# Optimization experiments

Hardware: AMD Instinct MI355X
Metric: run time of the kernel (lower is better)

## Reference

```python
import jax, jax.numpy as jnp
import numpy as np

B, T, D_MODEL = 2, 2048, 2048
Q_HEADS, KV_HEADS = 16, 4
HEAD_DIM = D_MODEL // Q_HEADS  # 128
N_GROUPS = Q_HEADS // KV_HEADS  # 4
THETA = 10000.0


def setup_inputs() -> dict:
    key = jax.random.key(0)
    ks = jax.random.split(key, 5)
    s = 0.02
    return {
        "x": jax.random.normal(ks[0], (B, T, D_MODEL), dtype=jnp.float32),
        "Wq": jax.random.normal(ks[1], (Q_HEADS * HEAD_DIM, D_MODEL), dtype=jnp.float32) * s,
        "Wk": jax.random.normal(ks[2], (KV_HEADS * HEAD_DIM, D_MODEL), dtype=jnp.float32) * s,
        "Wv": jax.random.normal(ks[3], (KV_HEADS * HEAD_DIM, D_MODEL), dtype=jnp.float32) * s,
        "Wo": jax.random.normal(ks[4], (D_MODEL, D_MODEL), dtype=jnp.float32) * s,
    }


def _apply_rope(q, k, t):
    # freqs = outer(arange(t), 1/theta^(2i/d)) ; complex rotation on (even,odd) pairs
    inv_freq = 1.0 / (THETA ** (jnp.arange(0, HEAD_DIM, 2, dtype=jnp.float32) / HEAD_DIM))
    ang = jnp.arange(t, dtype=jnp.float32)[:, None] * inv_freq[None, :]  # [t, hd/2]
    cos = jnp.cos(ang)[None, :, None, :]  # [1,t,1,hd/2]
    sin = jnp.sin(ang)[None, :, None, :]

    def rot(x):
        xr = x.reshape(*x.shape[:-1], HEAD_DIM // 2, 2)
        xe, xo = xr[..., 0], xr[..., 1]
        out = jnp.stack([xe * cos - xo * sin, xe * sin + xo * cos], axis=-1)
        return out.reshape(x.shape)

    return rot(q), rot(k)


def reference(x, Wq, Wk, Wv, Wo):
    b, t, c = x.shape
    q = (x @ Wq.T).reshape(b, t, Q_HEADS, HEAD_DIM)
    k = (x @ Wk.T).reshape(b, t, KV_HEADS, HEAD_DIM)
    v = (x @ Wv.T).reshape(b, t, KV_HEADS, HEAD_DIM)
    q, k = _apply_rope(q, k, t)
    # GQA: repeat kv heads to match q heads (repeat_interleave on head dim)
    k = jnp.repeat(k, N_GROUPS, axis=2)
    v = jnp.repeat(v, N_GROUPS, axis=2)
    q = q.transpose(0, 2, 1, 3)  # [b,h,t,d]
    k = k.transpose(0, 2, 1, 3)
    v = v.transpose(0, 2, 1, 3)
    scale = HEAD_DIM ** -0.5
    attn = jnp.einsum("bhqd,bhkd->bhqk", q, k) * scale
    causal = jnp.tril(jnp.ones((t, t), dtype=bool))
    attn = jnp.where(causal[None, None], attn, -jnp.inf)
    attn = jax.nn.softmax(attn, axis=-1)
    out = jnp.einsum("bhqk,bhkd->bhqd", attn, v)
    out = out.transpose(0, 2, 1, 3).reshape(b, t, c)
    return out @ Wo.T
```

## Files before the change

kernel.cpp:

```cpp
#include <hip/hip_runtime.h>
#include <hip/hip_bf16.h>

typedef __bf16 bf16_t;
typedef __bf16 bf16x8 __attribute__((ext_vector_type(8)));
typedef __bf16 bf16x4 __attribute__((ext_vector_type(4)));
typedef float f32x4 __attribute__((ext_vector_type(4)));

#define SEQ_T 2048
#define DMODEL 2048
#define NQH 16
#define NKVH 4
#define HDIM 128

__device__ __forceinline__ f32x4 mfma16x16x32(bf16x8 a, bf16x8 b, f32x4 c) {
  return __builtin_amdgcn_mfma_f32_16x16x32_bf16(a, b, c, 0, 0, 0);
}

typedef __attribute__((address_space(3))) void lds_void_t;
typedef __attribute__((address_space(1))) const void gbl_void_t;
__device__ __forceinline__ void gload_lds16(const bf16_t* g, bf16_t* l) {
  __builtin_amdgcn_global_load_lds((gbl_void_t*)g, (lds_void_t*)l, 16, 0, 0);
}
__device__ __forceinline__ void BAR() {
  asm volatile("" ::: "memory");
  __builtin_amdgcn_s_barrier();
  asm volatile("" ::: "memory");
}

__global__ __launch_bounds__(256) void cast_all(const float* __restrict__ x,
                                                const float* __restrict__ Wq,
                                                const float* __restrict__ Wk,
                                                const float* __restrict__ Wv,
                                                const float* __restrict__ Wo,
                                                bf16_t* __restrict__ xb,
                                                bf16_t* __restrict__ Wqkvb,
                                                bf16_t* __restrict__ Wob) {
  const int idx = blockIdx.x * 256 + threadIdx.x;
  const float* src;
  bf16_t* dst;
  if (idx < 1048576) {
    src = x + (size_t)idx * 8;
    dst = xb + (size_t)idx * 8;
  } else if (idx < 1572864) {
    const int r = idx - 1048576;
    src = Wq + (size_t)r * 8;
    dst = Wqkvb + (size_t)r * 8;
  } else if (idx < 1703936) {
    const int r = idx - 1572864;
    src = Wk + (size_t)r * 8;
    dst = Wqkvb + 4194304 + (size_t)r * 8;
  } else if (idx < 1835008) {
    const int r = idx - 1703936;
    src = Wv + (size_t)r * 8;
    dst = Wqkvb + 5242880 + (size_t)r * 8;
  } else {
    const int r = idx - 1835008;
    src = Wo + (size_t)r * 8;
    dst = Wob + (size_t)r * 8;
  }
  const float4* s4 = reinterpret_cast<const float4*>(src);
  float4 a = s4[0], b = s4[1];
  bf16x8 r8 = {(bf16_t)a.x, (bf16_t)a.y, (bf16_t)a.z, (bf16_t)a.w,
               (bf16_t)b.x, (bf16_t)b.y, (bf16_t)b.z, (bf16_t)b.w};
  *reinterpret_cast<bf16x8*>(dst) = r8;
}

__global__ __launch_bounds__(256) void sincos_kernel(float2* __restrict__ tab) {
  int idx = blockIdx.x * 256 + threadIdx.x;
  int t = idx >> 6, i = idx & 63;
  float inv = powf(10000.0f, -(float)i * (1.0f / 64.0f));
  float ang = (float)t * inv;
  float s, c;
  sincosf(ang, &s, &c);
  tab[idx] = make_float2(c, s);
}

__global__ __launch_bounds__(512, 2) void gemm_qkv(const bf16_t* __restrict__ A,
                                                   const bf16_t* __restrict__ W,
                                                   bf16_t* __restrict__ q_out,
                                                   bf16_t* __restrict__ k_out,
                                                   bf16_t* __restrict__ v_out,
                                                   const float2* __restrict__ tab) {
  constexpr int K = 2048;
  constexpr int NT = 32;
  const int id = ((int)blockIdx.x & 7) * 32 + ((int)blockIdx.x >> 3);
  const int m0 = (id >> 4) * 256, n0 = (id & 15) * 192;
  const int tid = threadIdx.x;
  const int lane = tid & 63, w = tid >> 6;
  const int wr = w >> 2, wc = w & 3;
  const int l15 = lane & 15, g = lane >> 4;
  __shared__ bf16_t smem[2][(256 + 192) * 64];
  f32x4 acc[8][3] = {};
  bf16x8 af[4][2], bfr[3][2];

  auto ISSUE_A = [&](int tt, int h) {
    bf16_t* base = &smem[tt & 1][0] + h * (128 * 64);
    const bf16_t* src = A + (size_t)(m0 + h * 128) * K + tt * 64;
#pragma unroll
    for (int i = 0; i < 2; i++) {
      const int rl = i * 64 + (tid >> 3);
      gload_lds16(src + (size_t)rl * K + (((tid & 7) ^ (rl & 7)) << 3),
                  base + (i * 64 + w * 8) * 64);
    }
  };
  auto ISSUE_B = [&](int tt, int c) {
    bf16_t* base = &smem[tt & 1][0] + (256 + c * 64) * 64;
    const int rl = tid >> 3;
    const bf16_t* src = W + (size_t)(n0 + c * 64 + rl) * K + tt * 64;
    gload_lds16(src + (((tid & 7) ^ (rl & 7)) << 3), base + (w * 8) * 64);
  };
  auto RDA = [&](const bf16_t* Ab, int qm) {
#pragma unroll
    for (int fi = 0; fi < 4; fi++) {
      const int row = wr * 128 + qm * 64 + fi * 16 + l15;
#pragma unroll
      for (int ksl = 0; ksl < 2; ksl++)
        af[fi][ksl] = *reinterpret_cast<const bf16x8*>(
            Ab + row * 64 + ((((ksl << 2) + g) ^ (row & 7)) << 3));
    }
  };
  auto RDB1 = [&](const bf16_t* Bb, int fj) {
    const int row = wc * 48 + fj * 16 + l15;
#pragma unroll
    for (int ksl = 0; ksl < 2; ksl++)
      bfr[fj][ksl] = *reinterpret_cast<const bf16x8*>(
          Bb + row * 64 + ((((ksl << 2) + g) ^ (row & 7)) << 3));
  };

#define MMX(QM, FJLO, FJHI)                                                   \
  do {                                                                        \
    __builtin_amdgcn_s_setprio(1);                                            \
    _Pragma("unroll") for (int fi = 0; fi < 4; fi++)                          \
        _Pragma("unroll") for (int fj = (FJLO); fj <= (FJHI); fj++)           \
            _Pragma("unroll") for (int ksl = 0; ksl < 2; ksl++)               \
                acc[(QM)*4 + fi][fj] =                                        \
                    mfma16x16x32(af[fi][ksl], bfr[fj][ksl], acc[(QM)*4 + fi][fj]); \
    __builtin_amdgcn_s_setprio(0);                                            \
  } while (0)

  ISSUE_A(0, 0);
  ISSUE_A(0, 1);
  ISSUE_B(0, 0);
  ISSUE_B(0, 1);
  ISSUE_B(0, 2);

  for (int t = 0; t < NT; t++) {
    const bf16_t* Ab = &smem[t & 1][0];
    const bf16_t* Bb = Ab + 256 * 64;
    if (t + 1 < NT) {
      ISSUE_A(t + 1, 0);
      asm volatile("s_waitcnt vmcnt(2)" ::: "memory");
    } else {
      asm volatile("s_waitcnt vmcnt(0)" ::: "memory");
    }
    BAR();
    RDA(Ab, 0);
    RDB1(Bb, 0);
    RDB1(Bb, 1);
    MMX(0, 0, 1);
    BAR();
    RDB1(Bb, 2);
    if (t + 1 < NT) ISSUE_A(t + 1, 1);
    BAR();
    MMX(0, 2, 2);
    BAR();
    RDA(Ab, 1);
    if (t + 1 < NT) {
      ISSUE_B(t + 1, 0);
      ISSUE_B(t + 1, 1);
    }
    BAR();
    MMX(1, 0, 1);
    BAR();
    if (t + 1 < NT) ISSUE_B(t + 1, 2);
    BAR();
    MMX(1, 2, 2);
    BAR();
  }
#undef MMX

#pragma unroll
  for (int fm = 0; fm < 8; fm++) {
    const int r0 = m0 + wr * 128 + fm * 16 + (g << 2);
    const int bb = r0 >> 11;
    const int tt = r0 & 2047;
#pragma unroll
    for (int fn = 0; fn < 3; fn++) {
      const int col = n0 + wc * 48 + fn * 16 + l15;
      const f32x4 v = acc[fm][fn];
      if (col < 2048) {
        const int dd = col & 127;
        const float2* tp = tab + (size_t)tt * 64 + (dd >> 1);
        bf16_t* dst = q_out + (((size_t)(bb * NQH + (col >> 7)) * SEQ_T + tt) * HDIM + dd);
#pragma unroll
        for (int i = 0; i < 4; i++) {
          float me = v[i];
          float ot = __shfl_xor(me, 1);
          float2 cs = tp[(size_t)i * 64];
          float r = (dd & 1) ? (me * cs.x + ot * cs.y) : (me * cs.x - ot * cs.y);
          dst[(size_t)i * HDIM] = (bf16_t)r;
        }
      } else if (col < 2560) {
        const int dd = col & 127;
        const float2* tp = tab + (size_t)tt * 64 + (dd >> 1);
        bf16_t* dst = k_out + (((size_t)(bb * NKVH + ((col - 2048) >> 7)) * SEQ_T + tt) * HDIM + dd);
#pragma unroll
        for (int i = 0; i < 4; i++) {
          float me = v[i];
          float ot = __shfl_xor(me, 1);
          float2 cs = tp[(size_t)i * 64];
          float r = (dd & 1) ? (me * cs.x + ot * cs.y) : (me * cs.x - ot * cs.y);
          dst[(size_t)i * HDIM] = (bf16_t)r;
        }
      } else {
        const int vc = col - 2560;
        const int hh = vc >> 7, dd = vc & 127;
        const int tp64 = (tt & ~63) | (((tt >> 2) & 3) << 4) | (((tt >> 4) & 3) << 2);
        bf16x4 pk = {(bf16_t)v[0], (bf16_t)v[1], (bf16_t)v[2], (bf16_t)v[3]};
        *reinterpret_cast<bf16x4*>(v_out + (((size_t)(bb * NKVH + hh) * HDIM + dd) * SEQ_T + tp64)) = pk;
      }
    }
  }
}

__global__ __launch_bounds__(512, 2) void gemm_out(const bf16_t* __restrict__ A,
                                                   const bf16_t* __restrict__ W,
                                                   float* __restrict__ c_out) {
  constexpr int K = 2048;
  constexpr int NT = 32;
  const int id = ((int)blockIdx.x & 7) * 32 + ((int)blockIdx.x >> 3);
  const int m0 = (id >> 4) * 256, n0 = (id & 15) * 128;
  const int tid = threadIdx.x;
  const int lane = tid & 63, w = tid >> 6;
  const int wr = w >> 2, wc = w & 3;
  const int l15 = lane & 15, g = lane >> 4;
  __shared__ bf16_t smem[2][(256 + 128) * 64];
  f32x4 acc[8][2] = {};
  bf16x8 af[4][2], bfr[1][2];

  auto ISSUE_HALF = [&](int tt, int h) {
    const int k0 = tt * 64;
    bf16_t* base = &smem[tt & 1][0] + ((h < 2) ? h * (128 * 64) : 256 * 64);
    const bf16_t* src = (h < 2) ? (A + (size_t)(m0 + h * 128) * K)
                                : (W + (size_t)n0 * K);
#pragma unroll
    for (int i = 0; i < 2; i++) {
      const int rl = i * 64 + (tid >> 3);
      gload_lds16(src + (size_t)rl * K + k0 + (((tid & 7) ^ (rl & 7)) << 3),
                  base + (i * 64 + w * 8) * 64);
    }
  };
  auto RDA = [&](const bf16_t* Ab, int qm) {
#pragma unroll
    for (int fi = 0; fi < 4; fi++) {
      const int row = wr * 128 + qm * 64 + fi * 16 + l15;
#pragma unroll
      for (int ksl = 0; ksl < 2; ksl++)
        af[fi][ksl] = *reinterpret_cast<const bf16x8*>(
            Ab + row * 64 + ((((ksl << 2) + g) ^ (row & 7)) << 3));
    }
  };
  auto RDB = [&](const bf16_t* Bb, int qn) {
    const int row = wc * 32 + qn * 16 + l15;
#pragma unroll
    for (int ksl = 0; ksl < 2; ksl++)
      bfr[0][ksl] = *reinterpret_cast<const bf16x8*>(
          Bb + row * 64 + ((((ksl << 2) + g) ^ (row & 7)) << 3));
  };

#define MMPH(QM, QN)                                                          \
  do {                                                                        \
    __builtin_amdgcn_s_setprio(1);                                            \
    _Pragma("unroll") for (int fi = 0; fi < 4; fi++)                          \
        _Pragma("unroll") for (int ksl = 0; ksl < 2; ksl++)                   \
            acc[(QM)*4 + fi][(QN)] =                                          \
                mfma16x16x32(af[fi][ksl], bfr[0][ksl], acc[(QM)*4 + fi][(QN)]); \
    __builtin_amdgcn_s_setprio(0);                                            \
  } while (0)

#pragma unroll
  for (int h = 0; h < 3; h++) ISSUE_HALF(0, h);

  for (int t = 0; t < NT; t++) {
    const bf16_t* Ab = &smem[t & 1][0];
    const bf16_t* Bb = Ab + 256 * 64;
    if (t + 1 < NT) {
      ISSUE_HALF(t + 1, 0);
      asm volatile("s_waitcnt vmcnt(2)" ::: "memory");
    } else {
      asm volatile("s_waitcnt vmcnt(0)" ::: "memory");
    }
    BAR();
    RDA(Ab, 0);
    RDB(Bb, 0);
    MMPH(0, 0);
    BAR();
    RDB(Bb, 1);
    if (t + 1 < NT) ISSUE_HALF(t + 1, 1);
    BAR();
    MMPH(0, 1);
    BAR();
    RDA(Ab, 1);
    if (t + 1 < NT) ISSUE_HALF(t + 1, 2);
    BAR();
    MMPH(1, 1);
    BAR();
    RDB(Bb, 0);
    BAR();
    MMPH(1, 0);
    BAR();
  }
#undef MMPH

#pragma unroll
  for (int fm = 0; fm < 8; fm++) {
    const int r0 = m0 + wr * 128 + fm * 16 + (g << 2);
#pragma unroll
    for (int fn = 0; fn < 2; fn++) {
      const int col = n0 + wc * 32 + fn * 16 + l15;
#pragma unroll
      for (int i = 0; i < 4; i++) c_out[(size_t)(r0 + i) * 2048 + col] = acc[fm][fn][i];
    }
  }
}

__global__ __launch_bounds__(256, 2) void attn_kernel(const bf16_t* __restrict__ Qb,
                                                      const bf16_t* __restrict__ Kb,
                                                      const bf16_t* __restrict__ Vt,
                                                      bf16_t* __restrict__ AO) {
  const int bh = blockIdx.x;
  const int b = bh >> 4, h = bh & 15, kvh = h >> 2;
  const int p = blockIdx.y;
  const int jH = 31 - p, jL = p;
  const int q0H = jH * 64, q0L = jL * 64;
  const int tid = threadIdx.x;
  const int lane = tid & 63, w = tid >> 6;
  const bf16_t* Qp = Qb + (size_t)(b * NQH + h) * SEQ_T * HDIM;
  const bf16_t* Kp = Kb + (size_t)(b * NKVH + kvh) * SEQ_T * HDIM;
  const bf16_t* Vp = Vt + (size_t)(b * NKVH + kvh) * HDIM * SEQ_T;
  __shared__ bf16_t smem[2][16384];
  const int l15 = lane & 15, g = lane >> 4;
  const int qrA = q0H + w * 16 + l15;
  const int qrB = q0L + w * 16 + l15;
  bf16x8 qfA[4], qfB[4];
#pragma unroll
  for (int c = 0; c < 4; c++) {
    qfA[c] = *reinterpret_cast<const bf16x8*>(Qp + (size_t)qrA * HDIM + c * 32 + (g << 3));
    qfB[c] = *reinterpret_cast<const bf16x8*>(Qp + (size_t)qrB * HDIM + c * 32 + (g << 3));
  }
  f32x4 oA[8] = {}, oB[8] = {};
  float mA = -1e30f, lA = 0.0f, mB = -1e30f, lB = 0.0f;
  const float kscale = 0.08838834764831845f * 1.4426950408889634f;
  const int wmaxB = q0L + w * 16 + 15;
  const int ntiles = jH + 1;

  auto STAGE = [&](int it, int buf) {
    const int kv0s = it * 64;
    bf16_t* Ks = smem[buf];
    bf16_t* Vs = smem[buf] + 8192;
#pragma unroll
    for (int cc = 0; cc < 4; cc++) {
      const int ck = cc * 256 + tid;
      const int krow = ck >> 4, kg = ck & 15;
      gload_lds16(Kp + (size_t)(kv0s + krow) * HDIM + ((kg ^ (krow & 7)) << 3),
                  Ks + (cc * 256 + w * 64) * 8);
      const int vrow = ck >> 3, vg = ck & 7;
      gload_lds16(Vp + (size_t)vrow * SEQ_T + kv0s + ((vg ^ (vrow & 7)) << 3),
                  Vs + (cc * 256 + w * 64) * 8);
    }
  };

  auto SOFTMAX = [&](float* sv, float& m, float& l, f32x4* o, bf16x8* pc) {
    float a0 = fmaxf(fmaxf(sv[0], sv[1]), fmaxf(sv[2], sv[3]));
    float a1 = fmaxf(fmaxf(sv[4], sv[5]), fmaxf(sv[6], sv[7]));
    float a2 = fmaxf(fmaxf(sv[8], sv[9]), fmaxf(sv[10], sv[11]));
    float a3 = fmaxf(fmaxf(sv[12], sv[13]), fmaxf(sv[14], sv[15]));
    float tm = fmaxf(fmaxf(a0, a1), fmaxf(a2, a3));
    tm = fmaxf(tm, __shfl_xor(tm, 16, 64));
    tm = fmaxf(tm, __shfl_xor(tm, 32, 64));
    tm *= kscale;
    if (!__all(tm <= m + 8.0f)) {
      const float mnew = fmaxf(m, tm);
      const float alpha = exp2f(m - mnew);
      m = mnew;
      l *= alpha;
#pragma unroll
      for (int dt = 0; dt < 8; dt++) o[dt] *= alpha;
    }
#pragma unroll
    for (int j = 0; j < 16; j++) sv[j] = exp2f(__builtin_fmaf(sv[j], kscale, -m));
    float r0 = (sv[0] + sv[1]) + (sv[2] + sv[3]);
    float r1 = (sv[4] + sv[5]) + (sv[6] + sv[7]);
    float r2 = (sv[8] + sv[9]) + (sv[10] + sv[11]);
    float r3 = (sv[12] + sv[13]) + (sv[14] + sv[15]);
    float rs = (r0 + r1) + (r2 + r3);
    rs += __shfl_xor(rs, 16, 64);
    rs += __shfl_xor(rs, 32, 64);
    l += rs;
#pragma unroll
    for (int s = 0; s < 2; s++) {
      bf16x8 t = {(bf16_t)sv[8 * s],     (bf16_t)sv[8 * s + 1], (bf16_t)sv[8 * s + 2],
                  (bf16_t)sv[8 * s + 3], (bf16_t)sv[8 * s + 4], (bf16_t)sv[8 * s + 5],
                  (bf16_t)sv[8 * s + 6], (bf16_t)sv[8 * s + 7]};
      pc[s] = t;
    }
  };

  auto COMPUTE1 = [&](const bf16_t* Ks, const bf16_t* Vs, int kv0) {
    float sv[16];
    const bool noMask = (kv0 + 63 <= q0H + w * 16);
    __builtin_amdgcn_s_setprio(1);
#pragma unroll
    for (int ksub = 0; ksub < 4; ksub++) {
      f32x4 sa = {};
      const int krow = ksub * 16 + l15;
#pragma unroll
      for (int ch = 0; ch < 4; ch++) {
        bf16x8 kf = *reinterpret_cast<const bf16x8*>(
            Ks + krow * 128 + ((((ch << 2) + g) ^ (krow & 7)) << 3));
        sa = mfma16x16x32(kf, qfA[ch], sa);
      }
      if (noMask) {
#pragma unroll
        for (int i = 0; i < 4; i++) sv[ksub * 4 + i] = sa[i];
      } else {
        const int dlt = qrA - kv0 - ksub * 16 - (g << 2);
#pragma unroll
        for (int i = 0; i < 4; i++) sv[ksub * 4 + i] = (i <= dlt) ? sa[i] : -3e38f;
      }
    }
    __builtin_amdgcn_s_setprio(0);
    bf16x8 pc[2];
    SOFTMAX(sv, mA, lA, oA, pc);
    __builtin_amdgcn_s_setprio(1);
#pragma unroll
    for (int dt = 0; dt < 8; dt++) {
      const int vrow = dt * 16 + l15;
#pragma unroll
      for (int s = 0; s < 2; s++) {
        bf16x8 vv = *reinterpret_cast<const bf16x8*>(
            Vs + vrow * 64 + (((2 * g + s) ^ (vrow & 7)) << 3));
        oA[dt] = mfma16x16x32(vv, pc[s], oA[dt]);
      }
    }
    __builtin_amdgcn_s_setprio(0);
  };

  auto COMPUTE2 = [&](const bf16_t* Ks, const bf16_t* Vs, int kv0) {
    float svA[16], svB[16];
    const bool noMaskB = (kv0 + 63 <= q0L + w * 16);
    __builtin_amdgcn_s_setprio(1);
#pragma unroll
    for (int ksub = 0; ksub < 4; ksub++) {
      f32x4 sa = {}, sb = {};
      const int krow = ksub * 16 + l15;
#pragma unroll
      for (int ch = 0; ch < 4; ch++) {
        bf16x8 kf = *reinterpret_cast<const bf16x8*>(
            Ks + krow * 128 + ((((ch << 2) + g) ^ (krow & 7)) << 3));
        sa = mfma16x16x32(kf, qfA[ch], sa);
        sb = mfma16x16x32(kf, qfB[ch], sb);
      }
#pragma unroll
      for (int i = 0; i < 4; i++) svA[ksub * 4 + i] = sa[i];
      if (noMaskB) {
#pragma unroll
        for (int i = 0; i < 4; i++) svB[ksub * 4 + i] = sb[i];
      } else {
        const int dltB = qrB - kv0 - ksub * 16 - (g << 2);
#pragma unroll
        for (int i = 0; i < 4; i++) svB[ksub * 4 + i] = (i <= dltB) ? sb[i] : -3e38f;
      }
    }
    __builtin_amdgcn_s_setprio(0);
    bf16x8 pcA[2], pcB[2];
    SOFTMAX(svA, mA, lA, oA, pcA);
    SOFTMAX(svB, mB, lB, oB, pcB);
    __builtin_amdgcn_s_setprio(1);
#pragma unroll
    for (int dt = 0; dt < 8; dt++) {
      const int vrow = dt * 16 + l15;
#pragma unroll
      for (int s = 0; s < 2; s++) {
        bf16x8 vv = *reinterpret_cast<const bf16x8*>(
            Vs + vrow * 64 + (((2 * g + s) ^ (vrow & 7)) << 3));
        oA[dt] = mfma16x16x32(vv, pcA[s], oA[dt]);
        oB[dt] = mfma16x16x32(vv, pcB[s], oB[dt]);
      }
    }
    __builtin_amdgcn_s_setprio(0);
  };

  STAGE(0, 0);
  for (int it = 0; it < ntiles; it++) {
    const int buf = it & 1;
    if (it + 1 < ntiles) {
      STAGE(it + 1, buf ^ 1);
      asm volatile("s_waitcnt vmcnt(8)" ::: "memory");
    } else {
      asm volatile("s_waitcnt vmcnt(0)" ::: "memory");
    }
    BAR();
    const int kv0 = it * 64;
    const bf16_t* Ks = smem[buf];
    const bf16_t* Vs = smem[buf] + 8192;
    if (kv0 <= wmaxB) {
      COMPUTE2(Ks, Vs, kv0);
    } else {
      COMPUTE1(Ks, Vs, kv0);
    }
    BAR();
  }
  bf16_t* os = &smem[0][0] + w * 2048;
  auto EPI = [&](f32x4* o, float lsum, int q0) {
    const float linv = 1.0f / lsum;
#pragma unroll
    for (int dt = 0; dt < 8; dt++) {
      bf16x4 pk = {(bf16_t)(o[dt][0] * linv), (bf16_t)(o[dt][1] * linv),
                   (bf16_t)(o[dt][2] * linv), (bf16_t)(o[dt][3] * linv)};
      *reinterpret_cast<bf16x4*>(os + l15 * 128 + dt * 16 + (g << 2)) = pk;
    }
    const size_t rowb = (size_t)b * SEQ_T + q0 + w * 16;
#pragma unroll
    for (int kk = 0; kk < 4; kk++) {
      const int c = lane + kk * 64;
      const int q = c >> 4, gc = c & 15;
      *reinterpret_cast<bf16x8*>(AO + (rowb + q) * DMODEL + h * HDIM + gc * 8) =
          *reinterpret_cast<const bf16x8*>(os + q * 128 + gc * 8);
    }
  };
  EPI(oA, lA, q0H);
  EPI(oB, lB, q0L);
}

extern "C" void kernel_launch(void* const* d_in, const int* in_sizes, int n_in,
                              void* d_out, int out_size, void* d_ws, size_t ws_size,
                              hipStream_t stream) {
  const float* x = (const float*)d_in[0];
  const float* Wq = (const float*)d_in[1];
  const float* Wk = (const float*)d_in[2];
  const float* Wv = (const float*)d_in[3];
  const float* Wo = (const float*)d_in[4];
  float* out = (float*)d_out;
  char* ws = (char*)d_ws;
  bf16_t* xb = (bf16_t*)(ws);
  bf16_t* Wqkvb = (bf16_t*)(ws + 16777216);
  bf16_t* Wob = (bf16_t*)(ws + 29360128);
  bf16_t* Qb = (bf16_t*)(ws + 37748736);
  bf16_t* Kb = (bf16_t*)(ws + 54525952);
  bf16_t* Vt = (bf16_t*)(ws + 58720256);
  bf16_t* AO = (bf16_t*)(ws + 62914560);
  float2* tab = (float2*)(ws + 79691776);

  cast_all<<<9216, 256, 0, stream>>>(x, Wq, Wk, Wv, Wo, xb, Wqkvb, Wob);
  sincos_kernel<<<512, 256, 0, stream>>>(tab);
  gemm_qkv<<<256, 512, 0, stream>>>(xb, Wqkvb, Qb, Kb, Vt, tab);
  attn_kernel<<<dim3(32, 16), 256, 0, stream>>>(Qb, Kb, Vt, AO);
  gemm_out<<<256, 512, 0, stream>>>(AO, Wob, out);
}
```

Baseline: 181.5 us.

## Pair GQA heads per attention block and issue GEMM prefetches earlier

Measured after the change: 186.1 us. +2.5%, slower.

```diff
diff --git a/kernel.cpp b/kernel.cpp
--- a/kernel.cpp
+++ b/kernel.cpp
@@ -68,7 +68,7 @@
 __global__ __launch_bounds__(256) void sincos_kernel(float2* __restrict__ tab) {
   int idx = blockIdx.x * 256 + threadIdx.x;
   int t = idx >> 6, i = idx & 63;
-  float inv = powf(10000.0f, -(float)i * (1.0f / 64.0f));
+  float inv = exp2f((float)i * (-13.287712379549449f / 64.0f));
   float ang = (float)t * inv;
   float s, c;
   sincosf(ang, &s, &c);
@@ -149,7 +149,8 @@
     const bf16_t* Bb = Ab + 256 * 64;
     if (t + 1 < NT) {
       ISSUE_A(t + 1, 0);
-      asm volatile("s_waitcnt vmcnt(2)" ::: "memory");
+      ISSUE_A(t + 1, 1);
+      asm volatile("s_waitcnt vmcnt(4)" ::: "memory");
     } else {
       asm volatile("s_waitcnt vmcnt(0)" ::: "memory");
     }
@@ -160,20 +161,17 @@
     MMX(0, 0, 1);
     BAR();
     RDB1(Bb, 2);
-    if (t + 1 < NT) ISSUE_A(t + 1, 1);
-    BAR();
-    MMX(0, 2, 2);
-    BAR();
-    RDA(Ab, 1);
     if (t + 1 < NT) {
       ISSUE_B(t + 1, 0);
       ISSUE_B(t + 1, 1);
-    }
+      ISSUE_B(t + 1, 2);
+    }
+    BAR();
+    MMX(0, 2, 2);
+    BAR();
+    RDA(Ab, 1);
     BAR();
     MMX(1, 0, 1);
-    BAR();
-    if (t + 1 < NT) ISSUE_B(t + 1, 2);
-    BAR();
     MMX(1, 2, 2);
     BAR();
   }
@@ -286,7 +284,8 @@
     const bf16_t* Bb = Ab + 256 * 64;
     if (t + 1 < NT) {
       ISSUE_HALF(t + 1, 0);
-      asm volatile("s_waitcnt vmcnt(2)" ::: "memory");
+      ISSUE_HALF(t + 1, 1);
+      asm volatile("s_waitcnt vmcnt(4)" ::: "memory");
     } else {
       asm volatile("s_waitcnt vmcnt(0)" ::: "memory");
     }
@@ -296,12 +295,11 @@
     MMPH(0, 0);
     BAR();
     RDB(Bb, 1);
-    if (t + 1 < NT) ISSUE_HALF(t + 1, 1);
+    if (t + 1 < NT) ISSUE_HALF(t + 1, 2);
     BAR();
     MMPH(0, 1);
     BAR();
     RDA(Ab, 1);
-    if (t + 1 < NT) ISSUE_HALF(t + 1, 2);
     BAR();
     MMPH(1, 1);
     BAR();
@@ -328,31 +326,32 @@
                                                       const bf16_t* __restrict__ Kb,
                                                       const bf16_t* __restrict__ Vt,
                                                       bf16_t* __restrict__ AO) {
-  const int bh = blockIdx.x;
-  const int b = bh >> 4, h = bh & 15, kvh = h >> 2;
-  const int p = blockIdx.y;
-  const int jH = 31 - p, jL = p;
-  const int q0H = jH * 64, q0L = jL * 64;
+  const int bx = blockIdx.x;
+  const int b = bx >> 3, hp = bx & 7;
+  const int h0 = hp << 1;
+  const int kvh = h0 >> 2;
+  const int by = blockIdx.y;
+  const int j = (by < 16) ? (31 - by) : (by - 16);
+  const int q0 = j * 64;
   const int tid = threadIdx.x;
   const int lane = tid & 63, w = tid >> 6;
-  const bf16_t* Qp = Qb + (size_t)(b * NQH + h) * SEQ_T * HDIM;
+  const int l15 = lane & 15, g = lane >> 4;
+  const bf16_t* Qp0 = Qb + (size_t)(b * NQH + h0) * SEQ_T * HDIM;
+  const bf16_t* Qp1 = Qp0 + (size_t)SEQ_T * HDIM;
   const bf16_t* Kp = Kb + (size_t)(b * NKVH + kvh) * SEQ_T * HDIM;
   const bf16_t* Vp = Vt + (size_t)(b * NKVH + kvh) * HDIM * SEQ_T;
   __shared__ bf16_t smem[2][16384];
-  const int l15 = lane & 15, g = lane >> 4;
-  const int qrA = q0H + w * 16 + l15;
-  const int qrB = q0L + w * 16 + l15;
+  const int qr = q0 + w * 16 + l15;
   bf16x8 qfA[4], qfB[4];
 #pragma unroll
   for (int c = 0; c < 4; c++) {
-    qfA[c] = *reinterpret_cast<const bf16x8*>(Qp + (size_t)qrA * HDIM + c * 32 + (g << 3));
-    qfB[c] = *reinterpret_cast<const bf16x8*>(Qp + (size_t)qrB * HDIM + c * 32 + (g << 3));
+    qfA[c] = *reinterpret_cast<const bf16x8*>(Qp0 + (size_t)qr * HDIM + c * 32 + (g << 3));
+    qfB[c] = *reinterpret_cast<const bf16x8*>(Qp1 + (size_t)qr * HDIM + c * 32 + (g << 3));
   }
   f32x4 oA[8] = {}, oB[8] = {};
   float mA = -1e30f, lA = 0.0f, mB = -1e30f, lB = 0.0f;
   const float kscale = 0.08838834764831845f * 1.4426950408889634f;
-  const int wmaxB = q0L + w * 16 + 15;
-  const int ntiles = jH + 1;
+  const int ntiles = j + 1;
 
   auto STAGE = [&](int it, int buf) {
     const int kv0s = it * 64;
@@ -388,7 +387,7 @@
       for (int dt = 0; dt < 8; dt++) o[dt] *= alpha;
     }
 #pragma unroll
-    for (int j = 0; j < 16; j++) sv[j] = exp2f(__builtin_fmaf(sv[j], kscale, -m));
+    for (int jj = 0; jj < 16; jj++) sv[jj] = exp2f(__builtin_fmaf(sv[jj], kscale, -m));
     float r0 = (sv[0] + sv[1]) + (sv[2] + sv[3]);
     float r1 = (sv[4] + sv[5]) + (sv[6] + sv[7]);
     float r2 = (sv[8] + sv[9]) + (sv[10] + sv[11]);
@@ -406,49 +405,9 @@
     }
   };
 
-  auto COMPUTE1 = [&](const bf16_t* Ks, const bf16_t* Vs, int kv0) {
-    float sv[16];
-    const bool noMask = (kv0 + 63 <= q0H + w * 16);
-    __builtin_amdgcn_s_setprio(1);
-#pragma unroll
-    for (int ksub = 0; ksub < 4; ksub++) {
-      f32x4 sa = {};
-      const int krow = ksub * 16 + l15;
-#pragma unroll
-      for (int ch = 0; ch < 4; ch++) {
-        bf16x8 kf = *reinterpret_cast<const bf16x8*>(
-            Ks + krow * 128 + ((((ch << 2) + g) ^ (krow & 7)) << 3));
-        sa = mfma16x16x32(kf, qfA[ch], sa);
-      }
-      if (noMask) {
-#pragma unroll
-        for (int i = 0; i < 4; i++) sv[ksub * 4 + i] = sa[i];
-      } else {
-        const int dlt = qrA - kv0 - ksub * 16 - (g << 2);
-#pragma unroll
-        for (int i = 0; i < 4; i++) sv[ksub * 4 + i] = (i <= dlt) ? sa[i] : -3e38f;
-      }
-    }
-    __builtin_amdgcn_s_setprio(0);
-    bf16x8 pc[2];
-    SOFTMAX(sv, mA, lA, oA, pc);
-    __builtin_amdgcn_s_setprio(1);
-#pragma unroll
-    for (int dt = 0; dt < 8; dt++) {
-      const int vrow = dt * 16 + l15;
-#pragma unroll
-      for (int s = 0; s < 2; s++) {
-        bf16x8 vv = *reinterpret_cast<const bf16x8*>(
-            Vs + vrow * 64 + (((2 * g + s) ^ (vrow & 7)) << 3));
-        oA[dt] = mfma16x16x32(vv, pc[s], oA[dt]);
-      }
-    }
-    __builtin_amdgcn_s_setprio(0);
-  };
-
-  auto COMPUTE2 = [&](const bf16_t* Ks, const bf16_t* Vs, int kv0) {
+  auto COMPUTE = [&](const bf16_t* Ks, const bf16_t* Vs, int kv0) {
     float svA[16], svB[16];
-    const bool noMaskB = (kv0 + 63 <= q0L + w * 16);
+    const bool noMask = (kv0 != q0);
     __builtin_amdgcn_s_setprio(1);
 #pragma unroll
     for (int ksub = 0; ksub < 4; ksub++) {
@@ -461,15 +420,16 @@
         sa = mfma16x16x32(kf, qfA[ch], sa);
         sb = mfma16x16x32(kf, qfB[ch], sb);
       }
-#pragma unroll
-      for (int i = 0; i < 4; i++) svA[ksub * 4 + i] = sa[i];
-      if (noMaskB) {
-#pragma unroll
-        for (int i = 0; i < 4; i++) svB[ksub * 4 + i] = sb[i];
+      if (noMask) {
+#pragma unroll
+        for (int i = 0; i < 4; i++) { svA[ksub * 4 + i] = sa[i]; svB[ksub * 4 + i] = sb[i]; }
       } else {
-        const int dltB = qrB - kv0 - ksub * 16 - (g << 2);
-#pragma unroll
-        for (int i = 0; i < 4; i++) svB[ksub * 4 + i] = (i <= dltB) ? sb[i] : -3e38f;
+        const int dlt = qr - kv0 - ksub * 16 - (g << 2);
+#pragma unroll
+        for (int i = 0; i < 4; i++) {
+          svA[ksub * 4 + i] = (i <= dlt) ? sa[i] : -3e38f;
+          svB[ksub * 4 + i] = (i <= dlt) ? sb[i] : -3e38f;
+        }
       }
     }
     __builtin_amdgcn_s_setprio(0);
@@ -501,18 +461,11 @@
       asm volatile("s_waitcnt vmcnt(0)" ::: "memory");
     }
     BAR();
-    const int kv0 = it * 64;
-    const bf16_t* Ks = smem[buf];
-    const bf16_t* Vs = smem[buf] + 8192;
-    if (kv0 <= wmaxB) {
-      COMPUTE2(Ks, Vs, kv0);
-    } else {
-      COMPUTE1(Ks, Vs, kv0);
-    }
+    COMPUTE(smem[buf], smem[buf] + 8192, it * 64);
     BAR();
   }
   bf16_t* os = &smem[0][0] + w * 2048;
-  auto EPI = [&](f32x4* o, float lsum, int q0) {
+  auto EPI = [&](f32x4* o, float lsum, int h) {
     const float linv = 1.0f / lsum;
 #pragma unroll
     for (int dt = 0; dt < 8; dt++) {
@@ -529,8 +482,8 @@
           *reinterpret_cast<const bf16x8*>(os + q * 128 + gc * 8);
     }
   };
-  EPI(oA, lA, q0H);
-  EPI(oB, lB, q0L);
+  EPI(oA, lA, h0);
+  EPI(oB, lB, h0 + 1);
 }
 
 extern "C" void kernel_launch(void* const* d_in, const int* in_sizes, int n_in,
@@ -555,6 +508,6 @@
   cast_all<<<9216, 256, 0, stream>>>(x, Wq, Wk, Wv, Wo, xb, Wqkvb, Wob);
   sincos_kernel<<<512, 256, 0, stream>>>(tab);
   gemm_qkv<<<256, 512, 0, stream>>>(xb, Wqkvb, Qb, Kb, Vt, tab);
-  attn_kernel<<<dim3(32, 16), 256, 0, stream>>>(Qb, Kb, Vt, AO);
+  attn_kernel<<<dim3(16, 32), 256, 0, stream>>>(Qb, Kb, Vt, AO);
   gemm_out<<<256, 512, 0, stream>>>(AO, Wob, out);
 }
```
